# Optimization experiments

Measured on AMD Instinct MI355X. Metric: run time of the kernel, lower is better.

The kernel has to match this reference:

```python
import jax, jax.numpy as jnp
import numpy as np

CROP_H = 14
CROP_W = 14
EXTRAP = 0.0  # extrapolation_value


def setup_inputs() -> dict:
    key = jax.random.key(0)
    k1, k2, k3 = jax.random.split(key, 3)
    image = jax.random.normal(k1, (8, 256, 200, 304), dtype=jnp.float32)
    boxes = jax.random.uniform(k2, (1000, 4), dtype=jnp.float32)  # normalized [y1,x1,y2,x2]
    box_indices = jax.random.randint(k3, (1000,), 0, 8, dtype=jnp.int32)
    return {"image": image, "boxes": boxes, "box_indices": box_indices}


def _sample_coords(lo, hi, size, crop_size, dtype):
    # TF crop_and_resize coordinate mapping (normalized box -> pixel coords)
    if crop_size > 1:
        step = (hi - lo) * (size - 1) / (crop_size - 1)            # [N]
        return lo[:, None] * (size - 1) + jnp.arange(crop_size, dtype=dtype) * step[:, None]  # [N, crop]
    else:
        return 0.5 * (lo + hi)[:, None] * (size - 1)


def _crop_and_resize(image, boxes, box_indices):
    B, C, H, W = image.shape
    dt = image.dtype
    y1, x1, y2, x2 = boxes[:, 0], boxes[:, 1], boxes[:, 2], boxes[:, 3]

    in_y = _sample_coords(y1, y2, H, CROP_H, dt)   # [N, CROP_H]
    in_x = _sample_coords(x1, x2, W, CROP_W, dt)   # [N, CROP_W]

    valid_y = (in_y >= 0) & (in_y <= H - 1)        # [N, CROP_H]
    valid_x = (in_x >= 0) & (in_x <= W - 1)        # [N, CROP_W]

    top_f = jnp.floor(in_y)
    left_f = jnp.floor(in_x)
    y_lerp = in_y - top_f                          # [N, CROP_H]
    x_lerp = in_x - left_f                         # [N, CROP_W]

    top = jnp.clip(top_f, 0, H - 1).astype(jnp.int32)
    bot = jnp.clip(jnp.ceil(in_y), 0, H - 1).astype(jnp.int32)
    left = jnp.clip(left_f, 0, W - 1).astype(jnp.int32)
    right = jnp.clip(jnp.ceil(in_x), 0, W - 1).astype(jnp.int32)

    b = box_indices[:, None, None]                 # [N,1,1]

    def gather(yi, xi):
        # advanced indexing: result [N, CROP_H, CROP_W, C]
        return image[b, :, yi[:, :, None], xi[:, None, :]]

    tl = gather(top, left)
    tr = gather(top, right)
    bl = gather(bot, left)
    br = gather(bot, right)

    xl = x_lerp[:, None, :, None]                  # [N,1,CROP_W,1]
    yl = y_lerp[:, :, None, None]                  # [N,CROP_H,1,1]
    top_v = tl + (tr - tl) * xl
    bot_v = bl + (br - bl) * xl
    out = top_v + (bot_v - top_v) * yl             # [N,CROP_H,CROP_W,C]

    valid = valid_y[:, :, None, None] & valid_x[:, None, :, None]
    out = jnp.where(valid, out, jnp.asarray(EXTRAP, dt))
    return jnp.transpose(out, (0, 3, 1, 2))        # [N, C, CROP_H, CROP_W]


def reference(image, boxes, box_indices):
    return _crop_and_resize(image, boxes, box_indices)
```

## Files before the change

### kernel.cpp

```cpp
#include <hip/hip_runtime.h>

#define CROP  14
#define POS   196
#define HH    200
#define WW    304
#define CC    256
#define NIMG  8
#define TR    6
#define NT    34
#define NBIN  (NIMG*NT)
#define TSZ   (7*WW)
#define CPB   8


__device__ __forceinline__ int top_row(float y1, float y2, int yy) {
    const float in_y = y1*199.0f + (float)yy*((y2-y1)*199.0f*(1.0f/13.0f));
    return (int)fminf(fmaxf(floorf(in_y), 0.0f), 199.0f);
}

__global__ __launch_bounds__(1024) void prep(
    const float* __restrict__ boxes, const int* __restrict__ bidx, int n_boxes,
    unsigned* __restrict__ counts, unsigned* __restrict__ offsets,
    unsigned* __restrict__ cursors)
{
    __shared__ unsigned scnt[NBIN];
    const int t = threadIdx.x;
    if (t < NBIN) scnt[t] = 0;
    __syncthreads();
    for (int n = t; n < n_boxes; n += 1024) {
        const float y1 = boxes[4*n+0], y2 = boxes[4*n+2];
        const int b = bidx[n];
        int prev = -1, yyLo = 0;
        for (int yy = 0; yy < 14; ++yy) {
            const int tile = top_row(y1, y2, yy) / TR;
            if (tile != prev) {
                if (prev >= 0) atomicAdd(&scnt[b*NT+prev], (unsigned)((yy-yyLo)*CROP));
                prev = tile; yyLo = yy;
            }
        }
        atomicAdd(&scnt[b*NT+prev], (unsigned)((14-yyLo)*CROP));
    }
    __syncthreads();
    if (t == 0) {
        unsigned acc = 0;
        for (int i = 0; i < NBIN; ++i) {
            const unsigned c = scnt[i];
            counts[i] = c; offsets[i] = acc; cursors[i] = acc; acc += c;
        }
    }
}

__global__ __launch_bounds__(256) void emit_desc(
    const float* __restrict__ boxes, const int* __restrict__ bidx,
    unsigned* __restrict__ cursors, int4* __restrict__ desc)
{
    __shared__ int rowSlot[14];
    const int n = blockIdx.x;
    const int t = threadIdx.x;
    const float y1 = boxes[4*n+0], x1 = boxes[4*n+1];
    const float y2 = boxes[4*n+2], x2 = boxes[4*n+3];
    const int b = bidx[n];

    if (t == 0) {
        int tiles[14];
        for (int yy = 0; yy < 14; ++yy) tiles[yy] = top_row(y1, y2, yy) / TR;
        for (int yy = 0; yy < 14; ++yy) {
            if (yy == 0 || tiles[yy] != tiles[yy-1]) {
                int hi = yy;
                while (hi+1 < 14 && tiles[hi+1] == tiles[yy]) ++hi;
                const unsigned base = atomicAdd(&cursors[b*NT + tiles[yy]],
                                                (unsigned)((hi-yy+1)*CROP));
                for (int r = yy; r <= hi; ++r) rowSlot[r] = (int)base + (r-yy)*CROP;
            }
        }
    }
    __syncthreads();

    if (t < POS) {
        const int yy = t / CROP, xx = t - yy*CROP;
        const float in_y = y1*199.0f + (float)yy*((y2-y1)*199.0f*(1.0f/13.0f));
        const float in_x = x1*303.0f + (float)xx*((x2-x1)*303.0f*(1.0f/13.0f));
        const float tf = floorf(in_y), lf = floorf(in_x);
        const int topc   = (int)fminf(fmaxf(tf,          0.0f), 199.0f);
        const int botc   = (int)fminf(fmaxf(ceilf(in_y), 0.0f), 199.0f);
        const int leftc  = (int)fminf(fmaxf(lf,          0.0f), 303.0f);
        const int rightc = (int)fminf(fmaxf(ceilf(in_x), 0.0f), 303.0f);
        const int tile = topc / TR;
        const int r0   = topc - tile*TR;
        const unsigned w0 = (unsigned)(r0*WW + leftc)
                          | ((unsigned)(rightc - leftc) << 13)
                          | ((unsigned)(botc - topc)    << 14)
                          | ((unsigned)((in_y >= 0.0f) & (in_y <= 199.0f) &
                                        (in_x >= 0.0f) & (in_x <= 303.0f)) << 15);
        int4 d;
        d.x = (int)w0;
        d.y = n*CC*POS + t;
        d.z = __float_as_int(in_x - lf);
        d.w = __float_as_int(in_y - tf);
        desc[rowSlot[yy] + xx] = d;
    }
}

__global__ __launch_bounds__(512) void crop_compute(
    const float*    __restrict__ image,
    const unsigned* __restrict__ counts,
    const unsigned* __restrict__ offsets,
    const int4*     __restrict__ desc,
    float*          __restrict__ out)
{
    __shared__ float tile[CPB * TSZ];
    const int c0  = blockIdx.x * CPB;
    const int bin = blockIdx.y;
    const int b   = bin / NT;
    const int tl  = bin - b * NT;
    const int t   = threadIdx.x;
    const int base = tl * TR;
    const int rows = (tl == NT-1) ? (HH - (NT-1)*TR) : (TR + 1);

    const int S    = (int)counts[bin];
    const int off0 = (int)offsets[bin];

    {
        const float* src = image + ((size_t)b*CC + (size_t)c0)*(size_t)(HH*WW)
                                 + (size_t)base*WW;
        const int nv = (rows * WW) >> 2;
        for (int i = t; i < nv; i += 512) {
            #pragma unroll
            for (int p = 0; p < CPB; ++p) {
                ((float4*)(tile + p*TSZ))[i] = ((const float4*)(src + p*HH*WW))[i];
            }
        }
    }
    __syncthreads();
    if (S == 0) return;

    const size_t cb0 = (size_t)c0 * POS;
    for (int k = t; k < S; k += 512) {
        const int4 d = desc[off0 + k];
        const unsigned w0 = (unsigned)d.x;
        const int off = (int)(w0 & 0x1FFFu);
        const int dx  = (int)((w0 >> 13) & 1u);
        const int dyw = ((w0 >> 14) & 1u) ? WW : 0;
        const float xl = __int_as_float(d.z);
        const float yl = __int_as_float(d.w);
        const float zmask = (w0 & 0x8000u) ? 1.0f : 0.0f;
        const size_t o = (size_t)(unsigned)d.y + cb0;

        #pragma unroll
        for (int p = 0; p < CPB; ++p) {
            const float* pp = tile + p*TSZ + off;
            const float tlv = pp[0];
            const float trv = pp[dx];
            const float blv = pp[dyw];
            const float brv = pp[dyw + dx];
            const float tv = tlv + (trv - tlv) * xl;
            const float bv = blv + (brv - blv) * xl;
            const float v  = (tv + (bv - tv) * yl) * zmask;
            out[o + (size_t)p * POS] = v;
        }
    }
}

extern "C" void kernel_launch(void* const* d_in, const int* in_sizes, int n_in,
                              void* d_out, int out_size, void* d_ws, size_t ws_size,
                              hipStream_t stream) {
    const float* image = (const float*)d_in[0];
    const float* boxes = (const float*)d_in[1];
    const int*   bidx  = (const int*)d_in[2];
    float*       out   = (float*)d_out;
    const int n_boxes = in_sizes[1] / 4;

    unsigned* counts  = (unsigned*)d_ws;
    unsigned* offsets = counts + NBIN;
    unsigned* cursors = counts + 2*NBIN;
    int4*     desc    = (int4*)((char*)d_ws + 4096);

    prep<<<dim3(1), dim3(1024), 0, stream>>>(boxes, bidx, n_boxes, counts, offsets, cursors);
    emit_desc<<<dim3(n_boxes), dim3(256), 0, stream>>>(boxes, bidx, cursors, desc);
    crop_compute<<<dim3(CC/CPB, NBIN), dim3(512), 0, stream>>>(image, counts, offsets, desc, out);
}
```

Before: 188.2 us.

## Loop blocks over bin chunks with register-prefetched next image tile

The compute kernel now launches a fixed number of bin chunks per channel group, and each block walks several consecutive row-tile bins. It loads the next bin's image tile into registers while computing the current bin from shared memory. Channels per block are halved to reduce shared memory and free registers for the prefetch. This aims to overlap global loads with interpolation and stores, at the cost of more register pressure and an extra barrier per bin.

```diff
diff --git a/kernel.cpp b/kernel.cpp
--- a/kernel.cpp
+++ b/kernel.cpp
@@ -10,7 +10,8 @@
 #define NT    34
 #define NBIN  (NIMG*NT)
 #define TSZ   (7*WW)
-#define CPB   8
+#define CPB   4
+#define NCHUNK 32
 
 
 __device__ __forceinline__ int top_row(float y1, float y2, int yy) {
@@ -109,54 +110,96 @@
     float*          __restrict__ out)
 {
     __shared__ float tile[CPB * TSZ];
-    const int c0  = blockIdx.x * CPB;
-    const int bin = blockIdx.y;
-    const int b   = bin / NT;
-    const int tl  = bin - b * NT;
-    const int t   = threadIdx.x;
-    const int base = tl * TR;
-    const int rows = (tl == NT-1) ? (HH - (NT-1)*TR) : (TR + 1);
-
-    const int S    = (int)counts[bin];
-    const int off0 = (int)offsets[bin];
+    const int c0    = blockIdx.x * CPB;
+    const int chunk = blockIdx.y;
+    const int bin0  = (NBIN * chunk) / NCHUNK;
+    const int bin1  = (NBIN * (chunk + 1)) / NCHUNK;
+    const int t     = threadIdx.x;
+    const size_t cb0 = (size_t)c0 * POS;
+
+    float4 r0a, r0b, r1a, r1b, r2a, r2b, r3a, r3b;
 
     {
+        const int bin = bin0;
+        const int b = bin / NT, tl = bin - b * NT;
+        const int rows = (tl == NT-1) ? (HH - (NT-1)*TR) : (TR + 1);
+        const int nvp = (rows * WW) >> 2;
         const float* src = image + ((size_t)b*CC + (size_t)c0)*(size_t)(HH*WW)
-                                 + (size_t)base*WW;
-        const int nv = (rows * WW) >> 2;
-        for (int i = t; i < nv; i += 512) {
-            #pragma unroll
-            for (int p = 0; p < CPB; ++p) {
-                ((float4*)(tile + p*TSZ))[i] = ((const float4*)(src + p*HH*WW))[i];
-            }
-        }
-    }
-    __syncthreads();
-    if (S == 0) return;
-
-    const size_t cb0 = (size_t)c0 * POS;
-    for (int k = t; k < S; k += 512) {
-        const int4 d = desc[off0 + k];
-        const unsigned w0 = (unsigned)d.x;
-        const int off = (int)(w0 & 0x1FFFu);
-        const int dx  = (int)((w0 >> 13) & 1u);
-        const int dyw = ((w0 >> 14) & 1u) ? WW : 0;
-        const float xl = __int_as_float(d.z);
-        const float yl = __int_as_float(d.w);
-        const float zmask = (w0 & 0x8000u) ? 1.0f : 0.0f;
-        const size_t o = (size_t)(unsigned)d.y + cb0;
-
-        #pragma unroll
-        for (int p = 0; p < CPB; ++p) {
-            const float* pp = tile + p*TSZ + off;
-            const float tlv = pp[0];
-            const float trv = pp[dx];
-            const float blv = pp[dyw];
-            const float brv = pp[dyw + dx];
-            const float tv = tlv + (trv - tlv) * xl;
-            const float bv = blv + (brv - blv) * xl;
-            const float v  = (tv + (bv - tv) * yl) * zmask;
-            out[o + (size_t)p * POS] = v;
+                                 + (size_t)(tl*TR)*WW;
+        const float4* s0 = (const float4*)(src);
+        const float4* s1 = (const float4*)(src +     HH*WW);
+        const float4* s2 = (const float4*)(src + 2 * HH*WW);
+        const float4* s3 = (const float4*)(src + 3 * HH*WW);
+        if (t < nvp)       { r0a = s0[t];     r1a = s1[t];     r2a = s2[t];     r3a = s3[t]; }
+        if (t + 512 < nvp) { r0b = s0[t+512]; r1b = s1[t+512]; r2b = s2[t+512]; r3b = s3[t+512]; }
+    }
+
+    for (int bin = bin0; bin < bin1; ++bin) {
+        const int b = bin / NT, tl = bin - b * NT;
+        const int rows = (tl == NT-1) ? (HH - (NT-1)*TR) : (TR + 1);
+        const int nvp = (rows * WW) >> 2;
+
+        __syncthreads();
+        {
+            float4* t0 = (float4*)(tile);
+            float4* t1 = (float4*)(tile +     TSZ);
+            float4* t2 = (float4*)(tile + 2 * TSZ);
+            float4* t3 = (float4*)(tile + 3 * TSZ);
+            if (t < nvp)       { t0[t]     = r0a; t1[t]     = r1a; t2[t]     = r2a; t3[t]     = r3a; }
+            if (t + 512 < nvp) { t0[t+512] = r0b; t1[t+512] = r1b; t2[t+512] = r2b; t3[t+512] = r3b; }
+        }
+        if (bin + 1 < bin1) {
+            const int nb = bin + 1;
+            const int b2 = nb / NT, tl2 = nb - b2 * NT;
+            const int rows2 = (tl2 == NT-1) ? (HH - (NT-1)*TR) : (TR + 1);
+            const int nvp2 = (rows2 * WW) >> 2;
+            const float* src2 = image + ((size_t)b2*CC + (size_t)c0)*(size_t)(HH*WW)
+                                      + (size_t)(tl2*TR)*WW;
+            const float4* s0 = (const float4*)(src2);
+            const float4* s1 = (const float4*)(src2 +     HH*WW);
+            const float4* s2 = (const float4*)(src2 + 2 * HH*WW);
+            const float4* s3 = (const float4*)(src2 + 3 * HH*WW);
+            if (t < nvp2)       { r0a = s0[t];     r1a = s1[t];     r2a = s2[t];     r3a = s3[t]; }
+            if (t + 512 < nvp2) { r0b = s0[t+512]; r1b = s1[t+512]; r2b = s2[t+512]; r3b = s3[t+512]; }
+        }
+        __syncthreads();
+
+        const int S    = (int)counts[bin];
+        const int off0 = (int)offsets[bin];
+        for (int k = t; k < S; k += 512) {
+            const int4 d = desc[off0 + k];
+            const unsigned w0 = (unsigned)d.x;
+            const int off = (int)(w0 & 0x1FFFu);
+            const int dx  = (int)((w0 >> 13) & 1u);
+            const int dyw = ((w0 >> 14) & 1u) ? WW : 0;
+            const float xl = __int_as_float(d.z);
+            const float yl = __int_as_float(d.w);
+            const float zmask = (w0 & 0x8000u) ? 1.0f : 0.0f;
+            const size_t o = (size_t)(unsigned)d.y + cb0;
+
+            const float* p0 = tile + off;
+            const float* p1 = p0 + TSZ;
+            const float* p2 = p0 + 2*TSZ;
+            const float* p3 = p0 + 3*TSZ;
+
+            const float tl0 = p0[0], tr0 = p0[dx], bl0 = p0[dyw], br0 = p0[dyw+dx];
+            const float tl1 = p1[0], tr1 = p1[dx], bl1 = p1[dyw], br1 = p1[dyw+dx];
+            const float tl2 = p2[0], tr2 = p2[dx], bl2 = p2[dyw], br2 = p2[dyw+dx];
+            const float tl3 = p3[0], tr3 = p3[dx], bl3 = p3[dyw], br3 = p3[dyw+dx];
+
+            const float tv0 = tl0 + (tr0 - tl0) * xl;
+            const float bv0 = bl0 + (br0 - bl0) * xl;
+            const float tv1 = tl1 + (tr1 - tl1) * xl;
+            const float bv1 = bl1 + (br1 - bl1) * xl;
+            const float tv2 = tl2 + (tr2 - tl2) * xl;
+            const float bv2 = bl2 + (br2 - bl2) * xl;
+            const float tv3 = tl3 + (tr3 - tl3) * xl;
+            const float bv3 = bl3 + (br3 - bl3) * xl;
+
+            out[o]         = (tv0 + (bv0 - tv0) * yl) * zmask;
+            out[o +   POS] = (tv1 + (bv1 - tv1) * yl) * zmask;
+            out[o + 2*POS] = (tv2 + (bv2 - tv2) * yl) * zmask;
+            out[o + 3*POS] = (tv3 + (bv3 - tv3) * yl) * zmask;
         }
     }
 }
@@ -177,5 +220,5 @@
 
     prep<<<dim3(1), dim3(1024), 0, stream>>>(boxes, bidx, n_boxes, counts, offsets, cursors);
     emit_desc<<<dim3(n_boxes), dim3(256), 0, stream>>>(boxes, bidx, cursors, desc);
-    crop_compute<<<dim3(CC/CPB, NBIN), dim3(512), 0, stream>>>(image, counts, offsets, desc, out);
-}
+    crop_compute<<<dim3(CC/CPB, NCHUNK), dim3(512), 0, stream>>>(image, counts, offsets, desc, out);
+}
```

New measurement: 262.8 us. +39.7%, slower.
